# Kernel optimization log

Hardware: AMD Instinct MI355X
Metric: run time of the kernel (lower is better)

## Reference

```python
import jax, jax.numpy as jnp
import numpy as np

B, S, E, H, D = 4, 2048, 1024, 16, 64


def setup_inputs() -> dict:
    key = jax.random.key(0)
    ks = jax.random.split(key, 10)
    s_in = 1.0 / np.sqrt(E)
    s_out = 1.0 / np.sqrt(H * D)
    return {
        "x": jax.random.normal(ks[0], (B, S, E), dtype=jnp.float32),
        "wq": jax.random.uniform(ks[1], (H, E, D), jnp.float32, -s_in, s_in),
        "bq": jax.random.uniform(ks[2], (H, D), jnp.float32, -s_in, s_in),
        "wk": jax.random.uniform(ks[3], (H, E, D), jnp.float32, -s_in, s_in),
        "bk": jax.random.uniform(ks[4], (H, D), jnp.float32, -s_in, s_in),
        "wv": jax.random.uniform(ks[5], (H, E, D), jnp.float32, -s_in, s_in),
        "bv": jax.random.uniform(ks[6], (H, D), jnp.float32, -s_in, s_in),
        "wo": jax.random.uniform(ks[7], (H * D, E), jnp.float32, -s_out, s_out),
        "bo": jax.random.uniform(ks[8], (E,), jnp.float32, -s_out, s_out),
    }


def reference(x, wq, bq, wk, bk, wv, bv, wo, bo):
    # Batched equivalent of the per-head Python loop: project all heads at once.
    q = jnp.einsum("bse,hed->bhsd", x, wq) + bq[None, :, None, :]
    k = jnp.einsum("bse,hed->bhsd", x, wk) + bk[None, :, None, :]
    v = jnp.einsum("bse,hed->bhsd", x, wv) + bv[None, :, None, :]
    scale = 1.0 / jnp.sqrt(jnp.asarray(D, dtype=x.dtype))
    scores = jnp.einsum("bhsd,bhtd->bhst", q, k) * scale  # [B,H,S,S]
    causal = jnp.tril(jnp.ones((S, S), dtype=bool))
    scores = jnp.where(causal[None, None], scores, jnp.asarray(-jnp.inf, x.dtype))
    p = jax.nn.softmax(scores, axis=-1)
    o = jnp.einsum("bhst,bhtd->bhsd", p, v)
    # concat heads along last dim (head order matches the torch cat order)
    o = jnp.transpose(o, (0, 2, 1, 3)).reshape(B, S, H * D)
    y = o @ wo + bo  # output projection; dropout is identity in eval
    return y
```

## Files before the change

kernel.cpp:

```cpp
#include <hip/hip_runtime.h>
#include <math.h>

#define B_ 4
#define S_ 2048
#define E_ 1024
#define H_ 16
#define D_ 64

using f32x4 = __attribute__((ext_vector_type(4))) float;
using s16x8 = __attribute__((ext_vector_type(8))) short;

__device__ __forceinline__ unsigned short f2bf(float f) {
    unsigned int u = __float_as_uint(f);
    u = (u + 0x7FFFu + ((u >> 16) & 1u)) >> 16;
    return (unsigned short)u;
}

__device__ __forceinline__ unsigned int pack_bf2(float lo, float hi) {
    const unsigned int ulo = __float_as_uint(lo) + 0x8000u;
    const unsigned int uhi = __float_as_uint(hi) + 0x8000u;
    return __builtin_amdgcn_perm(uhi, ulo, 0x07060302u);
}

__device__ __forceinline__ void load_lds16(const void* g, void* l) {
    __builtin_amdgcn_global_load_lds(
        (const __attribute__((address_space(1))) void*)g,
        (__attribute__((address_space(3))) void*)l, 16, 0, 0);
}

#define QSCALE 0.18033688011112042f

__global__ __launch_bounds__(256)
void cast_x(const float* __restrict__ in, unsigned short* __restrict__ out)
{
    const size_t idx = (size_t)blockIdx.x * 2048 + threadIdx.x * 8;
    const float4 v0 = *(const float4*)&in[idx];
    const float4 v1 = *(const float4*)&in[idx + 4];
    uint4 p;
    p.x = (unsigned)f2bf(v0.x) | ((unsigned)f2bf(v0.y) << 16);
    p.y = (unsigned)f2bf(v0.z) | ((unsigned)f2bf(v0.w) << 16);
    p.z = (unsigned)f2bf(v1.x) | ((unsigned)f2bf(v1.y) << 16);
    p.w = (unsigned)f2bf(v1.z) | ((unsigned)f2bf(v1.w) << 16);
    *(uint4*)&out[idx] = p;
}

__global__ __launch_bounds__(256)
void transpose_w(const float* __restrict__ wq, const float* __restrict__ wk,
                 const float* __restrict__ wv, const float* __restrict__ wo,
                 unsigned short* __restrict__ Wqkvt, unsigned short* __restrict__ Wot)
{
    __shared__ float T[64][68];
    const int z = blockIdx.z;
    const float* in;
    unsigned short* out;
    int inStride, r0, c0;
    if (z < 48) {
        if (blockIdx.y != 0) return;
        const int t = z >> 4, h = z & 15;
        const float* W = (t == 0) ? wq : ((t == 1) ? wk : wv);
        in = W + (size_t)h * (E_ * D_);
        inStride = 64;
        out = Wqkvt + (size_t)(t * 1024 + h * 64) * 1024;
        r0 = blockIdx.x * 64; c0 = 0;
    } else {
        in = wo; inStride = 1024;
        out = Wot;
        r0 = blockIdx.x * 64; c0 = blockIdx.y * 64;
    }
    const int tid = threadIdx.x;
    #pragma unroll
    for (int i = 0; i < 4; ++i) {
        const int e = tid + i * 256;
        const int row = e >> 4, c4 = e & 15;
        const float4 v = *(const float4*)&in[(size_t)(r0 + row) * inStride + c0 + c4 * 4];
        T[row][c4 * 4 + 0] = v.x; T[row][c4 * 4 + 1] = v.y;
        T[row][c4 * 4 + 2] = v.z; T[row][c4 * 4 + 3] = v.w;
    }
    __syncthreads();
    #pragma unroll
    for (int i = 0; i < 2; ++i) {
        const int e = tid + i * 256;
        const int c = e >> 3, ch = e & 7;
        unsigned short h8[8];
        #pragma unroll
        for (int j = 0; j < 8; ++j) h8[j] = f2bf(T[ch * 8 + j][c]);
        uint4 p;
        p.x = (unsigned)h8[0] | ((unsigned)h8[1] << 16);
        p.y = (unsigned)h8[2] | ((unsigned)h8[3] << 16);
        p.z = (unsigned)h8[4] | ((unsigned)h8[5] << 16);
        p.w = (unsigned)h8[6] | ((unsigned)h8[7] << 16);
        *(uint4*)&out[(size_t)(c0 + c) * 1024 + r0 + ch * 8] = p;
    }
}

template<int MODE>
__global__ __launch_bounds__(256)
void gemm_mfma(const unsigned short* __restrict__ A,
               const unsigned short* __restrict__ Bt,
               const float* __restrict__ bq, const float* __restrict__ bk,
               const float* __restrict__ bv, const float* __restrict__ bo,
               unsigned short* __restrict__ Qb, unsigned short* __restrict__ Kb,
               unsigned short* __restrict__ Vt, float* __restrict__ Cout)
{
    __shared__ short As[2][128 * 64];
    __shared__ short Bs[2][128 * 64];

    const int tid  = threadIdx.x;
    const int w    = tid >> 6, lane = tid & 63;
    const int g    = lane >> 4, l15 = lane & 15;
    const int wm   = w >> 1, wn = w & 1;
    const int mbase = blockIdx.x * 128;
    const int nbase = blockIdx.y * 128;

    const int srow8 = lane >> 3;
    const int pswz  = (lane & 7) ^ srow8;

    f32x4 acc[4][4];
    #pragma unroll
    for (int mt = 0; mt < 4; ++mt)
        #pragma unroll
        for (int nt = 0; nt < 4; ++nt)
            acc[mt][nt] = (f32x4){0.f, 0.f, 0.f, 0.f};

    const size_t aoff = (size_t)(mbase + srow8) * 1024 + pswz * 8;
    const size_t boff = (size_t)(nbase + srow8) * 1024 + pswz * 8;

    #pragma unroll
    for (int c = 0; c < 4; ++c) {
        const int R = w * 32 + c * 8;
        load_lds16(&A[aoff + (size_t)R * 1024], &As[0][R * 64]);
        load_lds16(&Bt[boff + (size_t)R * 1024], &Bs[0][R * 64]);
    }

    #pragma unroll 1
    for (int it = 0; it < 16; ++it) {
        const int cur = it & 1;
        __syncthreads();
        if (it + 1 < 16) {
            const int k1 = (it + 1) * 64;
            #pragma unroll
            for (int c = 0; c < 4; ++c) {
                const int R = w * 32 + c * 8;
                load_lds16(&A[aoff + (size_t)R * 1024 + k1], &As[1 - cur][R * 64]);
                load_lds16(&Bt[boff + (size_t)R * 1024 + k1], &Bs[1 - cur][R * 64]);
            }
        }
        #pragma unroll
        for (int ks = 0; ks < 2; ++ks) {
            const int qa = ((g + ks * 4) ^ (l15 & 7)) * 8;
            s16x8 af[4], bf[4];
            #pragma unroll
            for (int mt = 0; mt < 4; ++mt)
                af[mt] = *(const s16x8*)&As[cur][(wm * 64 + mt * 16 + l15) * 64 + qa];
            #pragma unroll
            for (int nt = 0; nt < 4; ++nt)
                bf[nt] = *(const s16x8*)&Bs[cur][(wn * 64 + nt * 16 + l15) * 64 + qa];
            #pragma unroll
            for (int mt = 0; mt < 4; ++mt)
                #pragma unroll
                for (int nt = 0; nt < 4; ++nt)
                    acc[mt][nt] = __builtin_amdgcn_mfma_f32_16x16x32_bf16(
                        af[mt], bf[nt], acc[mt][nt], 0, 0, 0);
        }
    }

    #pragma unroll
    for (int nt = 0; nt < 4; ++nt) {
        const int ncol = nbase + wn * 64 + nt * 16 + l15;
        if (MODE == 0) {
            const int t  = ncol >> 10;
            const int hh = (ncol >> 6) & 15;
            const int d  = ncol & 63;
            const float* bias = (t == 0) ? bq : ((t == 1) ? bk : bv);
            const float sc = (t == 0) ? QSCALE : 1.0f;
            const float bval = bias[hh * 64 + d];
            #pragma unroll
            for (int mt = 0; mt < 4; ++mt)
                #pragma unroll
                for (int r = 0; r < 4; ++r) {
                    const int m = mbase + wm * 64 + mt * 16 + g * 4 + r;
                    const int b = m >> 11, s = m & 2047;
                    const unsigned short val = f2bf((acc[mt][nt][r] + bval) * sc);
                    if (t == 2)
                        Vt[((size_t)(b * 16 + hh) * 64 + d) * 2048 + s] = val;
                    else {
                        unsigned short* Out = (t == 0) ? Qb : Kb;
                        Out[((size_t)(b * 16 + hh) * 2048 + s) * 64 + d] = val;
                    }
                }
        } else {
            const float bval = bo[ncol];
            #pragma unroll
            for (int mt = 0; mt < 4; ++mt)
                #pragma unroll
                for (int r = 0; r < 4; ++r) {
                    const int m = mbase + wm * 64 + mt * 16 + g * 4 + r;
                    Cout[(size_t)m * 1024 + ncol] = acc[mt][nt][r] + bval;
                }
        }
    }
}

#define LDK 72
__global__ __launch_bounds__(512, 2)
void attn_mfma(const unsigned short* __restrict__ Qb,
               const unsigned short* __restrict__ Kb,
               const unsigned short* __restrict__ Vt,
               unsigned short* __restrict__ O)
{
    __shared__ short Kls[2][64 * LDK];
    __shared__ short Vls[2][64 * LDK];
    __shared__ short Pls[8][16 * LDK];

    const int tid  = threadIdx.x;
    const int w    = tid >> 6;
    const int lane = tid & 63;
    const int g    = lane >> 4;
    const int l15  = lane & 15;
    const int j    = blockIdx.x;
    const int j2   = 15 - j;
    const int h    = blockIdx.y;
    const int b    = blockIdx.z;

    const size_t hb = (size_t)(b * 16 + h) * (2048 * 64);
    const int qH = j2 * 128 + w * 16;
    const int qL = j * 128 + w * 16;

    s16x8 aqH[2], aqL[2];
    {
        const int rh = qH + l15, rl = qL + l15;
        aqH[0] = *(const s16x8*)&Qb[hb + (size_t)rh * 64 + g * 8];
        aqH[1] = *(const s16x8*)&Qb[hb + (size_t)rh * 64 + 32 + g * 8];
        aqL[0] = *(const s16x8*)&Qb[hb + (size_t)rl * 64 + g * 8];
        aqL[1] = *(const s16x8*)&Qb[hb + (size_t)rl * 64 + 32 + g * 8];
    }

    float lsumH = 0.f, lsumL = 0.f;
    f32x4 OH[4], OL[4];
    #pragma unroll
    for (int nt = 0; nt < 4; ++nt) { OH[nt] = (f32x4){0.f,0.f,0.f,0.f}; OL[nt] = (f32x4){0.f,0.f,0.f,0.f}; }

    const int stages      = 32 - 2 * j;
    const int lightStages = 2 * j + 2;

    const int srow = tid >> 3, spart = tid & 7;
    uint4 kreg = *(const uint4*)&Kb[hb + (size_t)srow * 64 + spart * 8];
    uint4 vreg = *(const uint4*)&Vt[hb + (size_t)srow * 2048 + spart * 8];

    for (int t = 0; t < stages; ++t) {
        const int t0  = t * 64;
        const int buf = t & 1;
        *(uint4*)&Kls[buf][srow * LDK + spart * 8] = kreg;
        *(uint4*)&Vls[buf][srow * LDK + spart * 8] = vreg;
        if (t + 1 < stages) {
            kreg = *(const uint4*)&Kb[hb + (size_t)(t0 + 64 + srow) * 64 + spart * 8];
            vreg = *(const uint4*)&Vt[hb + (size_t)srow * 2048 + t0 + 64 + spart * 8];
        }
        __syncthreads();

        #pragma unroll
        for (int half = 0; half < 2; ++half) {
            if (half == 1 && t >= lightStages) break;
            const s16x8* aq   = (half == 0) ? aqH : aqL;
            const int qbase   = (half == 0) ? qH : qL;
            f32x4* Oacc       = (half == 0) ? OH : OL;

            f32x4 Sf[4];
            #pragma unroll
            for (int ct = 0; ct < 4; ++ct) {
                f32x4 acc = (f32x4){0.f, 0.f, 0.f, 0.f};
                const s16x8 bk0 = *(const s16x8*)&Kls[buf][(ct * 16 + l15) * LDK + g * 8];
                const s16x8 bk1 = *(const s16x8*)&Kls[buf][(ct * 16 + l15) * LDK + 32 + g * 8];
                acc = __builtin_amdgcn_mfma_f32_16x16x32_bf16(bk0, aq[0], acc, 0, 0, 0);
                acc = __builtin_amdgcn_mfma_f32_16x16x32_bf16(bk1, aq[1], acc, 0, 0, 0);
                Sf[ct] = acc;
            }

            if (t0 + 63 > qbase) {
                const int query = qbase + l15;
                #pragma unroll
                for (int ct = 0; ct < 4; ++ct) {
                    const int kbase = t0 + ct * 16 + g * 4;
                    #pragma unroll
                    for (int r = 0; r < 4; ++r)
                        if (kbase + r > query) Sf[ct][r] = -1e30f;
                }
            }

            float lacc = 0.f;
            #pragma unroll
            for (int ct = 0; ct < 4; ++ct) {
                #pragma unroll
                for (int r = 0; r < 4; ++r) Sf[ct][r] = exp2f(Sf[ct][r]);
                lacc += (Sf[ct][0] + Sf[ct][1]) + (Sf[ct][2] + Sf[ct][3]);
            }
            if (half == 0) lsumH += lacc; else lsumL += lacc;

            #pragma unroll
            for (int ct = 0; ct < 4; ++ct) {
                uint2 pw;
                pw.x = pack_bf2(Sf[ct][0], Sf[ct][1]);
                pw.y = pack_bf2(Sf[ct][2], Sf[ct][3]);
                *(uint2*)&Pls[w][l15 * LDK + ct * 16 + g * 4] = pw;
            }

            const s16x8 pf0 = *(const s16x8*)&Pls[w][l15 * LDK + g * 8];
            const s16x8 pf1 = *(const s16x8*)&Pls[w][l15 * LDK + 32 + g * 8];
            #pragma unroll
            for (int nt = 0; nt < 4; ++nt) {
                const s16x8 bv0 = *(const s16x8*)&Vls[buf][(nt * 16 + l15) * LDK + g * 8];
                const s16x8 bv1 = *(const s16x8*)&Vls[buf][(nt * 16 + l15) * LDK + 32 + g * 8];
                Oacc[nt] = __builtin_amdgcn_mfma_f32_16x16x32_bf16(bv0, pf0, Oacc[nt], 0, 0, 0);
                Oacc[nt] = __builtin_amdgcn_mfma_f32_16x16x32_bf16(bv1, pf1, Oacc[nt], 0, 0, 0);
            }
        }
    }

    lsumH += __shfl_xor(lsumH, 16);
    lsumH += __shfl_xor(lsumH, 32);
    lsumL += __shfl_xor(lsumL, 16);
    lsumL += __shfl_xor(lsumL, 32);
    const float invH = 1.0f / lsumH;
    const float invL = 1.0f / lsumL;

    #pragma unroll
    for (int half = 0; half < 2; ++half) {
        const f32x4* Oacc = (half == 0) ? OH : OL;
        const float  inv  = (half == 0) ? invH : invL;
        const int query   = ((half == 0) ? qH : qL) + l15;
        #pragma unroll
        for (int nt = 0; nt < 4; ++nt) {
            uint2 pk;
            pk.x = pack_bf2(Oacc[nt][0] * inv, Oacc[nt][1] * inv);
            pk.y = pack_bf2(Oacc[nt][2] * inv, Oacc[nt][3] * inv);
            *(uint2*)&O[(size_t)(b * 2048 + query) * 1024 + h * 64 + nt * 16 + g * 4] = pk;
        }
    }
}

extern "C" void kernel_launch(void* const* d_in, const int* in_sizes, int n_in,
                              void* d_out, int out_size, void* d_ws, size_t ws_size,
                              hipStream_t stream) {
    const float* x  = (const float*)d_in[0];
    const float* wq = (const float*)d_in[1];
    const float* bq = (const float*)d_in[2];
    const float* wk = (const float*)d_in[3];
    const float* bk = (const float*)d_in[4];
    const float* wv = (const float*)d_in[5];
    const float* bv = (const float*)d_in[6];
    const float* wo = (const float*)d_in[7];
    const float* bo = (const float*)d_in[8];
    float* out = (float*)d_out;

    const size_t hsz = (size_t)B_ * H_ * S_ * D_;
    unsigned short* xb    = (unsigned short*)d_ws;
    unsigned short* Wqkvt = xb + hsz;
    unsigned short* Wot   = Wqkvt + (size_t)3072 * 1024;
    unsigned short* Qb    = Wot + (size_t)1024 * 1024;
    unsigned short* Kb    = Qb + hsz;
    unsigned short* Vt    = Kb + hsz;
    unsigned short* Ob    = Vt + hsz;

    cast_x<<<4096, 256, 0, stream>>>(x, xb);
    transpose_w<<<dim3(16, 16, 49), 256, 0, stream>>>(wq, wk, wv, wo, Wqkvt, Wot);
    gemm_mfma<0><<<dim3(64, 24), 256, 0, stream>>>(
        xb, Wqkvt, bq, bk, bv, nullptr, Qb, Kb, Vt, nullptr);
    attn_mfma<<<dim3(8, H_, B_), 512, 0, stream>>>(Qb, Kb, Vt, Ob);
    gemm_mfma<1><<<dim3(64, 8), 256, 0, stream>>>(
        Ob, Wot, nullptr, nullptr, nullptr, bo, nullptr, nullptr, nullptr, out);
}
```

Baseline: 267.5 us.

## Retile GEMMs to 512-thread blocks with 4-stage BK=32 LDS pipeline

Reworks both projection GEMMs to use 8-wave blocks with larger tiles (256x192 for QKV, 128x256 for output). The K loop now uses 32-wide steps with a 4-buffer LDS ring, prefetching three stages ahead. Explicit vmcnt waits plus a single barrier per step replace the double-buffered syncthreads scheme, and MFMA issue priority is raised. The aim is to overlap global-to-LDS loads with compute better and raise per-block data reuse. The trade-offs are higher register and LDS pressure, and correctness now depends on the hand-counted vmcnt values.

New measurement: 308.9 us. 1.15x slower.

```diff
diff --git a/kernel.cpp b/kernel.cpp
--- a/kernel.cpp
+++ b/kernel.cpp
@@ -27,6 +27,8 @@
         (const __attribute__((address_space(1))) void*)g,
         (__attribute__((address_space(3))) void*)l, 16, 0, 0);
 }
+
+#define WAITV(n) asm volatile("s_waitcnt vmcnt(" #n ")" ::: "memory")
 
 #define QSCALE 0.18033688011112042f
 
@@ -94,7 +96,7 @@
 }
 
 template<int MODE>
-__global__ __launch_bounds__(256)
+__global__ __launch_bounds__(512, 2)
 void gemm_mfma(const unsigned short* __restrict__ A,
                const unsigned short* __restrict__ Bt,
                const float* __restrict__ bq, const float* __restrict__ bk,
@@ -102,71 +104,94 @@
                unsigned short* __restrict__ Qb, unsigned short* __restrict__ Kb,
                unsigned short* __restrict__ Vt, float* __restrict__ Cout)
 {
-    __shared__ short As[2][128 * 64];
-    __shared__ short Bs[2][128 * 64];
+    constexpr int BM  = (MODE == 0) ? 256 : 128;
+    constexpr int BN  = (MODE == 0) ? 192 : 256;
+    constexpr int MTF = BM / 32;
+    constexpr int NTF = BN / 64;
+    constexpr int RBA = BM / 16;
+    constexpr int RBB = BN / 16;
+    constexpr int NU  = RBA + RBB;
+
+    __shared__ short As[4][BM * 32];
+    __shared__ short Bs[4][BN * 32];
 
     const int tid  = threadIdx.x;
     const int w    = tid >> 6, lane = tid & 63;
     const int g    = lane >> 4, l15 = lane & 15;
-    const int wm   = w >> 1, wn = w & 1;
-    const int mbase = blockIdx.x * 128;
-    const int nbase = blockIdx.y * 128;
-
-    const int srow8 = lane >> 3;
-    const int pswz  = (lane & 7) ^ srow8;
-
-    f32x4 acc[4][4];
-    #pragma unroll
-    for (int mt = 0; mt < 4; ++mt)
-        #pragma unroll
-        for (int nt = 0; nt < 4; ++nt)
+    const int wm   = w >> 2, wn = w & 3;
+    const int mbase = blockIdx.x * BM;
+    const int nbase = blockIdx.y * BN;
+
+    const int srow4  = lane >> 2;
+    const int schunk = (lane & 3) ^ (srow4 & 3);
+    const size_t aoff = (size_t)(mbase + srow4) * 1024 + schunk * 8;
+    const size_t boff = (size_t)(nbase + srow4) * 1024 + schunk * 8;
+
+    f32x4 acc[MTF][NTF];
+    #pragma unroll
+    for (int mt = 0; mt < MTF; ++mt)
+        #pragma unroll
+        for (int nt = 0; nt < NTF; ++nt)
             acc[mt][nt] = (f32x4){0.f, 0.f, 0.f, 0.f};
 
-    const size_t aoff = (size_t)(mbase + srow8) * 1024 + pswz * 8;
-    const size_t boff = (size_t)(nbase + srow8) * 1024 + pswz * 8;
-
-    #pragma unroll
-    for (int c = 0; c < 4; ++c) {
-        const int R = w * 32 + c * 8;
-        load_lds16(&A[aoff + (size_t)R * 1024], &As[0][R * 64]);
-        load_lds16(&Bt[boff + (size_t)R * 1024], &Bs[0][R * 64]);
-    }
+    auto STAGE = [&](int t, int buf) {
+        const int k0 = t * 32;
+        #pragma unroll
+        for (int i = 0; i < (NU + 7) / 8; ++i) {
+            const int u = w + i * 8;
+            if (NU % 8 != 0 && u >= NU) continue;
+            if (u < RBA) {
+                load_lds16(&A[aoff + (size_t)(u * 16) * 1024 + k0],
+                           &As[buf][u * 512]);
+            } else {
+                const int v = u - RBA;
+                load_lds16(&Bt[boff + (size_t)(v * 16) * 1024 + k0],
+                           &Bs[buf][v * 512]);
+            }
+        }
+    };
+
+    STAGE(0, 0); STAGE(1, 1); STAGE(2, 2);
+
+    const int qa = (g ^ (l15 & 3)) * 8;
 
     #pragma unroll 1
-    for (int it = 0; it < 16; ++it) {
-        const int cur = it & 1;
-        __syncthreads();
-        if (it + 1 < 16) {
-            const int k1 = (it + 1) * 64;
-            #pragma unroll
-            for (int c = 0; c < 4; ++c) {
-                const int R = w * 32 + c * 8;
-                load_lds16(&A[aoff + (size_t)R * 1024 + k1], &As[1 - cur][R * 64]);
-                load_lds16(&Bt[boff + (size_t)R * 1024 + k1], &Bs[1 - cur][R * 64]);
-            }
-        }
-        #pragma unroll
-        for (int ks = 0; ks < 2; ++ks) {
-            const int qa = ((g + ks * 4) ^ (l15 & 7)) * 8;
-            s16x8 af[4], bf[4];
-            #pragma unroll
-            for (int mt = 0; mt < 4; ++mt)
-                af[mt] = *(const s16x8*)&As[cur][(wm * 64 + mt * 16 + l15) * 64 + qa];
-            #pragma unroll
-            for (int nt = 0; nt < 4; ++nt)
-                bf[nt] = *(const s16x8*)&Bs[cur][(wn * 64 + nt * 16 + l15) * 64 + qa];
-            #pragma unroll
-            for (int mt = 0; mt < 4; ++mt)
-                #pragma unroll
-                for (int nt = 0; nt < 4; ++nt)
-                    acc[mt][nt] = __builtin_amdgcn_mfma_f32_16x16x32_bf16(
-                        af[mt], bf[nt], acc[mt][nt], 0, 0, 0);
-        }
-    }
-
-    #pragma unroll
-    for (int nt = 0; nt < 4; ++nt) {
-        const int ncol = nbase + wn * 64 + nt * 16 + l15;
+    for (int t = 0; t < 32; ++t) {
+        if (t < 30) {
+            if constexpr (MODE == 0) { if (w < 4) WAITV(8); else WAITV(6); }
+            else                     WAITV(6);
+        } else if (t == 30) {
+            if constexpr (MODE == 0) { if (w < 4) WAITV(4); else WAITV(3); }
+            else                     WAITV(3);
+        } else {
+            WAITV(0);
+        }
+        __builtin_amdgcn_s_barrier();
+
+        if (t < 29) STAGE(t + 3, (t + 3) & 3);
+
+        const int buf = t & 3;
+        s16x8 af[MTF], bf[NTF];
+        #pragma unroll
+        for (int mt = 0; mt < MTF; ++mt)
+            af[mt] = *(const s16x8*)&As[buf][(wm * (BM / 2) + mt * 16 + l15) * 32 + qa];
+        #pragma unroll
+        for (int nt = 0; nt < NTF; ++nt)
+            bf[nt] = *(const s16x8*)&Bs[buf][(wn * (BN / 4) + nt * 16 + l15) * 32 + qa];
+
+        __builtin_amdgcn_s_setprio(1);
+        #pragma unroll
+        for (int mt = 0; mt < MTF; ++mt)
+            #pragma unroll
+            for (int nt = 0; nt < NTF; ++nt)
+                acc[mt][nt] = __builtin_amdgcn_mfma_f32_16x16x32_bf16(
+                    af[mt], bf[nt], acc[mt][nt], 0, 0, 0);
+        __builtin_amdgcn_s_setprio(0);
+    }
+
+    #pragma unroll
+    for (int nt = 0; nt < NTF; ++nt) {
+        const int ncol = nbase + wn * (BN / 4) + nt * 16 + l15;
         if (MODE == 0) {
             const int t  = ncol >> 10;
             const int hh = (ncol >> 6) & 15;
@@ -175,10 +200,10 @@
             const float sc = (t == 0) ? QSCALE : 1.0f;
             const float bval = bias[hh * 64 + d];
             #pragma unroll
-            for (int mt = 0; mt < 4; ++mt)
+            for (int mt = 0; mt < MTF; ++mt)
                 #pragma unroll
                 for (int r = 0; r < 4; ++r) {
-                    const int m = mbase + wm * 64 + mt * 16 + g * 4 + r;
+                    const int m = mbase + wm * (BM / 2) + mt * 16 + g * 4 + r;
                     const int b = m >> 11, s = m & 2047;
                     const unsigned short val = f2bf((acc[mt][nt][r] + bval) * sc);
                     if (t == 2)
@@ -191,10 +216,10 @@
         } else {
             const float bval = bo[ncol];
             #pragma unroll
-            for (int mt = 0; mt < 4; ++mt)
+            for (int mt = 0; mt < MTF; ++mt)
                 #pragma unroll
                 for (int r = 0; r < 4; ++r) {
-                    const int m = mbase + wm * 64 + mt * 16 + g * 4 + r;
+                    const int m = mbase + wm * (BM / 2) + mt * 16 + g * 4 + r;
                     Cout[(size_t)m * 1024 + ncol] = acc[mt][nt][r] + bval;
                 }
         }
@@ -363,9 +388,9 @@
 
     cast_x<<<4096, 256, 0, stream>>>(x, xb);
     transpose_w<<<dim3(16, 16, 49), 256, 0, stream>>>(wq, wk, wv, wo, Wqkvt, Wot);
-    gemm_mfma<0><<<dim3(64, 24), 256, 0, stream>>>(
+    gemm_mfma<0><<<dim3(32, 16), 512, 0, stream>>>(
         xb, Wqkvt, bq, bk, bv, nullptr, Qb, Kb, Vt, nullptr);
     attn_mfma<<<dim3(8, H_, B_), 512, 0, stream>>>(Qb, Kb, Vt, Ob);
-    gemm_mfma<1><<<dim3(64, 8), 256, 0, stream>>>(
+    gemm_mfma<1><<<dim3(64, 4), 512, 0, stream>>>(
         Ob, Wot, nullptr, nullptr, nullptr, bo, nullptr, nullptr, nullptr, out);
 }
```

## Deepen GEMM pipeline to three LDS stages with 128x256 tiles and 512 threads

Applied to the files above, without the earlier changes.

Rewrites the projection GEMM kernel to use 512-thread blocks computing 128x256 output tiles, with a triple-buffered LDS pipeline that prefetches two K-steps ahead. Waits use explicit vmcnt counts and split barriers, and MFMA bursts run at raised priority. Loads for the next stages are interleaved between the two MFMA halves of each step. The aim is to hide global-memory latency and improve data reuse, at the cost of more LDS per block (about 144 KB) and fewer blocks in the grid.

Measured after the change: 271.8 us. No clear change (+1.6%).

```diff
diff --git a/kernel.cpp b/kernel.cpp
--- a/kernel.cpp
+++ b/kernel.cpp
@@ -27,6 +27,8 @@
         (const __attribute__((address_space(1))) void*)g,
         (__attribute__((address_space(3))) void*)l, 16, 0, 0);
 }
+
+#define WAITV(n) asm volatile("s_waitcnt vmcnt(" #n ")" ::: "memory")
 
 #define QSCALE 0.18033688011112042f
 
@@ -94,7 +96,7 @@
 }
 
 template<int MODE>
-__global__ __launch_bounds__(256)
+__global__ __launch_bounds__(512, 2)
 void gemm_mfma(const unsigned short* __restrict__ A,
                const unsigned short* __restrict__ Bt,
                const float* __restrict__ bq, const float* __restrict__ bk,
@@ -102,18 +104,20 @@
                unsigned short* __restrict__ Qb, unsigned short* __restrict__ Kb,
                unsigned short* __restrict__ Vt, float* __restrict__ Cout)
 {
-    __shared__ short As[2][128 * 64];
-    __shared__ short Bs[2][128 * 64];
+    __shared__ short As[3][128 * 64];
+    __shared__ short Bs[3][256 * 64];
 
     const int tid  = threadIdx.x;
     const int w    = tid >> 6, lane = tid & 63;
     const int g    = lane >> 4, l15 = lane & 15;
-    const int wm   = w >> 1, wn = w & 1;
+    const int wm   = w >> 2, wn = w & 3;
     const int mbase = blockIdx.x * 128;
-    const int nbase = blockIdx.y * 128;
-
-    const int srow8 = lane >> 3;
-    const int pswz  = (lane & 7) ^ srow8;
+    const int nbase = blockIdx.y * 256;
+
+    const int srow   = lane >> 3;
+    const int schunk = (lane & 7) ^ srow;
+    const size_t aoff = (size_t)(mbase + srow) * 1024 + schunk * 8;
+    const size_t boff = (size_t)(nbase + srow) * 1024 + schunk * 8;
 
     f32x4 acc[4][4];
     #pragma unroll
@@ -122,57 +126,85 @@
         for (int nt = 0; nt < 4; ++nt)
             acc[mt][nt] = (f32x4){0.f, 0.f, 0.f, 0.f};
 
-    const size_t aoff = (size_t)(mbase + srow8) * 1024 + pswz * 8;
-    const size_t boff = (size_t)(nbase + srow8) * 1024 + pswz * 8;
-
-    #pragma unroll
-    for (int c = 0; c < 4; ++c) {
-        const int R = w * 32 + c * 8;
-        load_lds16(&A[aoff + (size_t)R * 1024], &As[0][R * 64]);
-        load_lds16(&Bt[boff + (size_t)R * 1024], &Bs[0][R * 64]);
-    }
+    auto STAGE_A = [&](int t, int buf, int i) {
+        const int u = w * 2 + i;
+        load_lds16(&A[aoff + (size_t)(u * 8) * 1024 + t * 64], &As[buf][u * 512]);
+    };
+    auto STAGE_B = [&](int t, int buf, int i) {
+        const int u = w * 4 + i;
+        load_lds16(&Bt[boff + (size_t)(u * 8) * 1024 + t * 64], &Bs[buf][u * 512]);
+    };
+
+    STAGE_A(0, 0, 0); STAGE_A(0, 0, 1);
+    STAGE_B(0, 0, 0); STAGE_B(0, 0, 1); STAGE_B(0, 0, 2); STAGE_B(0, 0, 3);
+    STAGE_A(1, 1, 0); STAGE_A(1, 1, 1);
+    STAGE_B(1, 1, 0); STAGE_B(1, 1, 1); STAGE_B(1, 1, 2); STAGE_B(1, 1, 3);
+
+    const int pr = l15 & 7;
 
     #pragma unroll 1
-    for (int it = 0; it < 16; ++it) {
-        const int cur = it & 1;
-        __syncthreads();
-        if (it + 1 < 16) {
-            const int k1 = (it + 1) * 64;
-            #pragma unroll
-            for (int c = 0; c < 4; ++c) {
-                const int R = w * 32 + c * 8;
-                load_lds16(&A[aoff + (size_t)R * 1024 + k1], &As[1 - cur][R * 64]);
-                load_lds16(&Bt[boff + (size_t)R * 1024 + k1], &Bs[1 - cur][R * 64]);
-            }
-        }
-        #pragma unroll
-        for (int ks = 0; ks < 2; ++ks) {
-            const int qa = ((g + ks * 4) ^ (l15 & 7)) * 8;
-            s16x8 af[4], bf[4];
+    for (int t = 0; t < 16; ++t) {
+        const int buf = t % 3;
+        const int nb  = (t + 2) % 3;
+        if (t < 15) { WAITV(6); } else { WAITV(0); }
+        __builtin_amdgcn_s_barrier();
+        __builtin_amdgcn_sched_barrier(0);
+
+        s16x8 af[4], bf[4];
+
+        {
+            const int pc = (g ^ pr) * 8;
             #pragma unroll
             for (int mt = 0; mt < 4; ++mt)
-                af[mt] = *(const s16x8*)&As[cur][(wm * 64 + mt * 16 + l15) * 64 + qa];
+                af[mt] = *(const s16x8*)&As[buf][(wm * 64 + mt * 16 + l15) * 64 + pc];
             #pragma unroll
             for (int nt = 0; nt < 4; ++nt)
-                bf[nt] = *(const s16x8*)&Bs[cur][(wn * 64 + nt * 16 + l15) * 64 + qa];
+                bf[nt] = *(const s16x8*)&Bs[buf][(wn * 64 + nt * 16 + l15) * 64 + pc];
+        }
+        if (t + 2 < 16) { STAGE_A(t + 2, nb, 0); STAGE_A(t + 2, nb, 1); STAGE_B(t + 2, nb, 0); }
+        __builtin_amdgcn_s_barrier();
+        __builtin_amdgcn_sched_barrier(0);
+        __builtin_amdgcn_s_setprio(1);
+        #pragma unroll
+        for (int mt = 0; mt < 4; ++mt)
+            #pragma unroll
+            for (int nt = 0; nt < 4; ++nt)
+                acc[mt][nt] = __builtin_amdgcn_mfma_f32_16x16x32_bf16(
+                    af[mt], bf[nt], acc[mt][nt], 0, 0, 0);
+        __builtin_amdgcn_s_setprio(0);
+        __builtin_amdgcn_s_barrier();
+
+        {
+            const int pc = ((4 + g) ^ pr) * 8;
             #pragma unroll
             for (int mt = 0; mt < 4; ++mt)
-                #pragma unroll
-                for (int nt = 0; nt < 4; ++nt)
-                    acc[mt][nt] = __builtin_amdgcn_mfma_f32_16x16x32_bf16(
-                        af[mt], bf[nt], acc[mt][nt], 0, 0, 0);
-        }
+                af[mt] = *(const s16x8*)&As[buf][(wm * 64 + mt * 16 + l15) * 64 + pc];
+            #pragma unroll
+            for (int nt = 0; nt < 4; ++nt)
+                bf[nt] = *(const s16x8*)&Bs[buf][(wn * 64 + nt * 16 + l15) * 64 + pc];
+        }
+        if (t + 2 < 16) { STAGE_B(t + 2, nb, 1); STAGE_B(t + 2, nb, 2); STAGE_B(t + 2, nb, 3); }
+        __builtin_amdgcn_s_barrier();
+        __builtin_amdgcn_sched_barrier(0);
+        __builtin_amdgcn_s_setprio(1);
+        #pragma unroll
+        for (int mt = 0; mt < 4; ++mt)
+            #pragma unroll
+            for (int nt = 0; nt < 4; ++nt)
+                acc[mt][nt] = __builtin_amdgcn_mfma_f32_16x16x32_bf16(
+                    af[mt], bf[nt], acc[mt][nt], 0, 0, 0);
+        __builtin_amdgcn_s_setprio(0);
     }
 
     #pragma unroll
     for (int nt = 0; nt < 4; ++nt) {
         const int ncol = nbase + wn * 64 + nt * 16 + l15;
         if (MODE == 0) {
-            const int t  = ncol >> 10;
+            const int tt = ncol >> 10;
             const int hh = (ncol >> 6) & 15;
             const int d  = ncol & 63;
-            const float* bias = (t == 0) ? bq : ((t == 1) ? bk : bv);
-            const float sc = (t == 0) ? QSCALE : 1.0f;
+            const float* bias = (tt == 0) ? bq : ((tt == 1) ? bk : bv);
+            const float sc = (tt == 0) ? QSCALE : 1.0f;
             const float bval = bias[hh * 64 + d];
             #pragma unroll
             for (int mt = 0; mt < 4; ++mt)
@@ -181,10 +213,10 @@
                     const int m = mbase + wm * 64 + mt * 16 + g * 4 + r;
                     const int b = m >> 11, s = m & 2047;
                     const unsigned short val = f2bf((acc[mt][nt][r] + bval) * sc);
-                    if (t == 2)
+                    if (tt == 2)
                         Vt[((size_t)(b * 16 + hh) * 64 + d) * 2048 + s] = val;
                     else {
-                        unsigned short* Out = (t == 0) ? Qb : Kb;
+                        unsigned short* Out = (tt == 0) ? Qb : Kb;
                         Out[((size_t)(b * 16 + hh) * 2048 + s) * 64 + d] = val;
                     }
                 }
@@ -363,9 +395,9 @@
 
     cast_x<<<4096, 256, 0, stream>>>(x, xb);
     transpose_w<<<dim3(16, 16, 49), 256, 0, stream>>>(wq, wk, wv, wo, Wqkvt, Wot);
-    gemm_mfma<0><<<dim3(64, 24), 256, 0, stream>>>(
+    gemm_mfma<0><<<dim3(64, 12), 512, 0, stream>>>(
         xb, Wqkvt, bq, bk, bv, nullptr, Qb, Kb, Vt, nullptr);
     attn_mfma<<<dim3(8, H_, B_), 512, 0, stream>>>(Qb, Kb, Vt, Ob);
-    gemm_mfma<1><<<dim3(64, 8), 256, 0, stream>>>(
+    gemm_mfma<1><<<dim3(64, 4), 512, 0, stream>>>(
         Ob, Wot, nullptr, nullptr, nullptr, bo, nullptr, nullptr, nullptr, out);
 }
```
